# Kernel optimization log

Measured on AMD Instinct MI355X. Metric: run time of the kernel, lower is better.

The kernel has to match this reference:

```python
import jax, jax.numpy as jnp
import numpy as np

B = 16384
NUM_INPUTS = 256
ACTION_DIM = 16
H0 = 1024
H1 = 1024
K = 128  # num_support
MIN_BIN_WIDTH = 0.001
MIN_BIN_HEIGHT = 0.001
MIN_DERIVATIVE = 0.001
EDGE_CONST = float(np.log(np.exp(1.0 - 0.001) - 1.0))  # log(exp(0.999)-1)
LN_EPS = 1e-5


def setup_inputs() -> dict:
    key = jax.random.key(0)
    ks = jax.random.split(key, 16)
    def lin(kw, kb, fan_out, fan_in):
        w = 1.0 / np.sqrt(fan_in)
        W = jax.random.uniform(kw, (fan_out, fan_in), jnp.float32, -w, w)
        b = jax.random.uniform(kb, (fan_out,), jnp.float32, -w, w)
        return W, b
    w1, b1 = lin(ks[0], ks[1], H0, NUM_INPUTS)
    w2, b2 = lin(ks[2], ks[3], H1, H0 + ACTION_DIM)
    wv, bv = lin(ks[4], ks[5], 3 * K - 1, H1)
    wa = jax.random.uniform(ks[6], (1, H1), jnp.float32, -0.003, 0.003)
    ba = jax.random.uniform(ks[7], (1,), jnp.float32, -0.0003, 0.0003)
    wb = jax.random.uniform(ks[8], (1, H1), jnp.float32, -0.003, 0.003)
    bb = jax.random.uniform(ks[9], (1,), jnp.float32, -0.0003, 0.0003)
    return {
        "inputs": jax.random.normal(ks[10], (B, NUM_INPUTS), jnp.float32),
        "actions": jax.random.normal(ks[11], (B, ACTION_DIM), jnp.float32),
        "w1": w1, "b1": b1,
        "ln1_g": jnp.ones((H0,), jnp.float32), "ln1_b": jnp.zeros((H0,), jnp.float32),
        "w2": w2, "b2": b2,
        "ln2_g": jnp.ones((H1,), jnp.float32), "ln2_b": jnp.zeros((H1,), jnp.float32),
        "wv": wv, "bv": bv,
        "wa": wa, "ba": ba,
        "wb": wb, "bb": bb,
    }


def _layernorm(x, g, b):
    mu = jnp.mean(x, axis=-1, keepdims=True)
    var = jnp.mean((x - mu) ** 2, axis=-1, keepdims=True)
    return (x - mu) / jnp.sqrt(var + LN_EPS) * g + b


def reference(inputs, actions, w1, b1, ln1_g, ln1_b, w2, b2, ln2_g, ln2_b,
              wv, bv, wa, ba, wb, bb):
    # trunk MLP
    x = jax.nn.relu(_layernorm(inputs @ w1.T + b1, ln1_g, ln1_b))
    x = jnp.concatenate([x, actions], axis=1)
    x = jax.nn.relu(_layernorm(x @ w2.T + b2, ln2_g, ln2_b))

    spline_param = x @ wv.T + bv            # [B, 3K-1]
    scale_a = jnp.exp(x @ wa.T + ba)        # [B, 1]
    scale_b = x @ wb.T + bb                 # [B, 1]

    W = spline_param[:, :K]
    H = spline_param[:, K:2 * K]
    Draw = spline_param[:, 2 * K:]          # [B, K-1]

    W = MIN_BIN_WIDTH + (1 - MIN_BIN_WIDTH * K) * jax.nn.softmax(W, axis=1)
    H = MIN_BIN_HEIGHT + (1 - MIN_BIN_HEIGHT * K) * jax.nn.softmax(H, axis=1)
    Dmid = MIN_DERIVATIVE + jax.nn.softplus(Draw)
    edge = jnp.full((W.shape[0], 1), EDGE_CONST, W.dtype)
    D = jnp.concatenate([edge, Dmid, edge], axis=-1)  # [B, K+1]

    zeros = jnp.zeros((W.shape[0], 1), W.dtype)
    cumwidths = jnp.concatenate([zeros, jnp.cumsum(W, axis=-1)], axis=-1)
    cumwidths = cumwidths.at[..., -1].set(1.0)        # [B, K+1]
    widths = cumwidths[..., 1:] - cumwidths[..., :-1]

    cumheights = jnp.concatenate([zeros, jnp.cumsum(H, axis=-1)], axis=-1)
    cumheights = scale_a * cumheights + scale_b       # [B, K+1]
    heights = cumheights[..., 1:] - cumheights[..., :-1]

    tau = (jnp.arange(K, dtype=W.dtype) + 0.5) / K    # [K]

    # brute-force searchsorted: sum(tau >= cumwidths) - 1
    bin_idx = jnp.sum(tau[None, :, None] >= cumwidths[:, None, :], axis=-1) - 1  # [B,K]

    gather = lambda t: jnp.take_along_axis(t, bin_idx, axis=-1)
    input_cumwidths = gather(cumwidths)
    input_bin_widths = gather(widths)
    input_cumheights = gather(cumheights)
    input_heights = gather(heights)
    delta = heights / widths
    input_delta = gather(delta)
    input_derivatives = gather(D)
    input_derivatives_plus_one = gather(D[..., 1:])

    theta = (tau[None, :] - input_cumwidths) / input_bin_widths
    theta_one_minus = theta * (1 - theta)
    numerator = input_heights * (input_delta * theta ** 2 + input_derivatives * theta_one_minus)
    denominator = input_delta + (input_derivatives + input_derivatives_plus_one - 2 * input_delta) * theta_one_minus
    return input_cumheights + numerator / denominator  # [B, K]
```

## Files before the change

### kernel.cpp

```cpp
#include <hip/hip_runtime.h>
#include <hip/hip_bf16.h>
#include <math.h>

#define BROWS      16384
#define LN_EPS_F   1e-5f
#define MINW       0.001f
#define MINH       0.001f
#define MIND       0.001f
#define EDGE_CONST_F 0.5397423505783211f

typedef __bf16 bf16x8 __attribute__((ext_vector_type(8)));
typedef float  f32x4  __attribute__((ext_vector_type(4)));

__device__ __forceinline__ ushort f2bf(float x) {
    union { float f; unsigned u; } v; v.f = x;
    unsigned u = v.u;
    u += 0x7fffu + ((u >> 16) & 1u);
    return (ushort)(u >> 16);
}
__device__ __forceinline__ float bf2f(ushort h) {
    union { unsigned u; float f; } v; v.u = ((unsigned)h) << 16;
    return v.f;
}

__global__ __launch_bounds__(256, 2)
void gemm_bf16x3(const ushort* __restrict__ Ah, const ushort* __restrict__ Al,
                 const ushort* __restrict__ Bh, const ushort* __restrict__ Bl,
                 const float* __restrict__ bias,
                 float* __restrict__ C, int ldc, int Nstore, int Kpad)
{
    __shared__ ushort lds[32768];
    const int tid  = threadIdx.x;
    const int wid  = tid >> 6;
    const int lane = tid & 63;
    const int bm0  = blockIdx.x * 128;
    const int bn0  = blockIdx.y * 128;
    const int wm   = wid >> 1;
    const int wn   = wid & 1;
    const int l15  = lane & 15;
    const int kg   = lane >> 4;

    const ushort* gsrc[8];
    {
        const ushort* pb[4] = {Ah, Al, Bh, Bl};
        #pragma unroll
        for (int i = 0; i < 8; ++i) {
            const int F     = i * 4096 + tid * 16;
            const int pl    = F >> 13;
            const int chunk = (F & 8191) >> 4;
            const int kgrp  = chunk >> 7;
            const int row   = chunk & 127;
            const int r0    = (pl < 2) ? bm0 : bn0;
            gsrc[i] = pb[pl] + (size_t)(r0 + row) * Kpad + kgrp * 8;
        }
    }
    #define STAGE(bufbase, kelem)                                              \
        _Pragma("unroll")                                                      \
        for (int i = 0; i < 8; ++i) {                                          \
            __builtin_amdgcn_global_load_lds(                                  \
                (const __attribute__((address_space(1))) void*)(gsrc[i] + (kelem)), \
                (__attribute__((address_space(3))) void*)(&lds[(bufbase) + i * 2048 + wid * 512]), \
                16, 0, 0);                                                     \
        }

    f32x4 acc[4][4];
    #pragma unroll
    for (int m = 0; m < 4; ++m)
        #pragma unroll
        for (int n = 0; n < 4; ++n)
            acc[m][n] = (f32x4){0.f, 0.f, 0.f, 0.f};

    const int aoff = kg * 1024 + (wm * 64 + l15) * 8;
    const int boff = 8192 + kg * 1024 + (wn * 64 + l15) * 8;
    const int nt = Kpad >> 5;

    STAGE(0, 0);
    __syncthreads();
    int cur = 0;

    for (int t = 0; t < nt; ++t) {
        const int nxt = cur ^ 1;
        if (t + 1 < nt) STAGE(nxt * 16384, (t + 1) * 32);

        const int cb = cur * 16384;
        bf16x8 aH[4], aL[4], bH[4], bL[4];
        #pragma unroll
        for (int m = 0; m < 4; ++m) {
            aH[m] = *(const bf16x8*)&lds[cb + aoff + m * 128];
            aL[m] = *(const bf16x8*)&lds[cb + 4096 + aoff + m * 128];
        }
        #pragma unroll
        for (int n = 0; n < 4; ++n) {
            bH[n] = *(const bf16x8*)&lds[cb + boff + n * 128];
            bL[n] = *(const bf16x8*)&lds[cb + 4096 + boff + n * 128];
        }

        __builtin_amdgcn_s_setprio(1);
        #pragma unroll
        for (int m = 0; m < 4; ++m)
            #pragma unroll
            for (int n = 0; n < 4; ++n)
                acc[m][n] = __builtin_amdgcn_mfma_f32_16x16x32_bf16(aH[m], bH[n], acc[m][n], 0, 0, 0);
        #pragma unroll
        for (int m = 0; m < 4; ++m)
            #pragma unroll
            for (int n = 0; n < 4; ++n)
                acc[m][n] = __builtin_amdgcn_mfma_f32_16x16x32_bf16(aH[m], bL[n], acc[m][n], 0, 0, 0);
        #pragma unroll
        for (int m = 0; m < 4; ++m)
            #pragma unroll
            for (int n = 0; n < 4; ++n)
                acc[m][n] = __builtin_amdgcn_mfma_f32_16x16x32_bf16(aL[m], bH[n], acc[m][n], 0, 0, 0);
        __builtin_amdgcn_s_setprio(0);

        __syncthreads();
        cur = nxt;
    }
    #undef STAGE

    #pragma unroll
    for (int n = 0; n < 4; ++n) {
        const int col = bn0 + wn * 64 + n * 16 + l15;
        if (col < Nstore) {
            const float bs = bias[col];
            #pragma unroll
            for (int m = 0; m < 4; ++m) {
                const int row = bm0 + wm * 64 + m * 16 + kg * 4;
                #pragma unroll
                for (int r = 0; r < 4; ++r)
                    C[(size_t)(row + r) * ldc + col] = acc[m][n][r] + bs;
            }
        }
    }
}

__global__ __launch_bounds__(256)
void ln_relu_split(const float* __restrict__ Y,
                   const float* __restrict__ g, const float* __restrict__ b,
                   ushort* __restrict__ Xh, ushort* __restrict__ Xl, int xstride,
                   const float* __restrict__ actions, int dopad)
{
    __shared__ float red[4];
    const int row = blockIdx.x;
    const int tid = threadIdx.x;
    const float* y = Y + (size_t)row * 1024;

    const float4 v = *(const float4*)(y + tid * 4);
    float s = v.x + v.y + v.z + v.w;
    #pragma unroll
    for (int off = 32; off > 0; off >>= 1) s += __shfl_down(s, off, 64);
    if ((tid & 63) == 0) red[tid >> 6] = s;
    __syncthreads();
    const float mu = (red[0] + red[1] + red[2] + red[3]) * (1.f / 1024.f);
    __syncthreads();
    const float d0 = v.x - mu, d1 = v.y - mu, d2 = v.z - mu, d3 = v.w - mu;
    float s2 = d0 * d0 + d1 * d1 + d2 * d2 + d3 * d3;
    #pragma unroll
    for (int off = 32; off > 0; off >>= 1) s2 += __shfl_down(s2, off, 64);
    if ((tid & 63) == 0) red[tid >> 6] = s2;
    __syncthreads();
    const float var = (red[0] + red[1] + red[2] + red[3]) * (1.f / 1024.f);
    const float inv = 1.0f / sqrtf(var + LN_EPS_F);

    float o0 = fmaxf(0.f, d0 * inv * g[tid * 4 + 0] + b[tid * 4 + 0]);
    float o1 = fmaxf(0.f, d1 * inv * g[tid * 4 + 1] + b[tid * 4 + 1]);
    float o2 = fmaxf(0.f, d2 * inv * g[tid * 4 + 2] + b[tid * 4 + 2]);
    float o3 = fmaxf(0.f, d3 * inv * g[tid * 4 + 3] + b[tid * 4 + 3]);

    ushort4 oh, ol;
    oh.x = f2bf(o0); ol.x = f2bf(o0 - bf2f(oh.x));
    oh.y = f2bf(o1); ol.y = f2bf(o1 - bf2f(oh.y));
    oh.z = f2bf(o2); ol.z = f2bf(o2 - bf2f(oh.z));
    oh.w = f2bf(o3); ol.w = f2bf(o3 - bf2f(oh.w));
    *(ushort4*)(Xh + (size_t)row * xstride + tid * 4) = oh;
    *(ushort4*)(Xl + (size_t)row * xstride + tid * 4) = ol;

    if (actions != nullptr && tid < 16) {
        const float a = actions[(size_t)row * 16 + tid];
        const ushort h = f2bf(a);
        Xh[(size_t)row * xstride + 1024 + tid] = h;
        Xl[(size_t)row * xstride + 1024 + tid] = f2bf(a - bf2f(h));
    }
    if (dopad && tid >= 16 && tid < 64) {
        Xh[(size_t)row * xstride + 1024 + tid] = 0;
        Xl[(size_t)row * xstride + 1024 + tid] = 0;
    }
}

__global__ __launch_bounds__(256)
void split_mat(const float* __restrict__ src, int scols,
               ushort* __restrict__ Dh, ushort* __restrict__ Dl,
               int dcols, int total)
{
    const int idx = blockIdx.x * 256 + threadIdx.x;
    if (idx >= total) return;
    const int r = idx / dcols, c = idx % dcols;
    const float v = (c < scols) ? src[(size_t)r * scols + c] : 0.f;
    const ushort h = f2bf(v);
    Dh[idx] = h;
    Dl[idx] = f2bf(v - bf2f(h));
}

__global__ __launch_bounds__(256)
void build_wcat_split(const float* __restrict__ wv, const float* __restrict__ wa,
                      const float* __restrict__ wb, const float* __restrict__ bv,
                      const float* __restrict__ ba, const float* __restrict__ bb,
                      ushort* __restrict__ Wh, ushort* __restrict__ Wl,
                      float* __restrict__ bcat)
{
    const int idx = blockIdx.x * 256 + threadIdx.x;
    if (idx < 512 * 1024) {
        const int n = idx >> 10, k = idx & 1023;
        const float v = (n < 383) ? wv[n * 1024 + k]
                       : (n == 383) ? wa[k]
                       : (n == 384) ? wb[k] : 0.f;
        const ushort h = f2bf(v);
        Wh[idx] = h;
        Wl[idx] = f2bf(v - bf2f(h));
    }
    if (idx < 512) {
        bcat[idx] = (idx < 383) ? bv[idx] : (idx == 383) ? ba[0]
                   : (idx == 384) ? bb[0] : 0.f;
    }
}

__device__ __forceinline__ float softplus_f(float x) {
    return (x > 20.f) ? x : log1pf(expf(x));
}

__global__ __launch_bounds__(256)
void spline_rq(const float* __restrict__ P, float* __restrict__ Out)
{
    __shared__ float cw[4][132];
    __shared__ float ch[4][132];
    __shared__ float Dv[4][132];
    const int wid  = threadIdx.x >> 6;
    const int lane = threadIdx.x & 63;
    const int r    = blockIdx.x * 4 + wid;
    const float* p = P + (size_t)r * 385;
    const int e0 = 2 * lane, e1 = 2 * lane + 1;

    const float sa = expf(p[383]);
    const float sb = p[384];

    const float w0 = p[e0], w1 = p[e1];
    float mx = fmaxf(w0, w1);
    #pragma unroll
    for (int off = 1; off < 64; off <<= 1) mx = fmaxf(mx, __shfl_xor(mx, off, 64));
    const float xw0 = expf(w0 - mx), xw1 = expf(w1 - mx);
    float sw = xw0 + xw1;
    #pragma unroll
    for (int off = 1; off < 64; off <<= 1) sw += __shfl_xor(sw, off, 64);
    const float cwn = (1.f - MINW * 128.f) / sw;
    const float Wv0 = MINW + cwn * xw0;
    const float Wv1 = MINW + cwn * xw1;
    float s = Wv0 + Wv1;
    #pragma unroll
    for (int off = 1; off < 64; off <<= 1) {
        const float t = __shfl_up(s, off, 64);
        if (lane >= off) s += t;
    }
    if (lane == 0) cw[wid][0] = 0.f;
    cw[wid][e1]     = s - Wv1;
    cw[wid][e1 + 1] = (lane == 63) ? 1.0f : s;

    const float h0 = p[128 + e0], h1 = p[128 + e1];
    float mh = fmaxf(h0, h1);
    #pragma unroll
    for (int off = 1; off < 64; off <<= 1) mh = fmaxf(mh, __shfl_xor(mh, off, 64));
    const float xh0 = expf(h0 - mh), xh1 = expf(h1 - mh);
    float sh = xh0 + xh1;
    #pragma unroll
    for (int off = 1; off < 64; off <<= 1) sh += __shfl_xor(sh, off, 64);
    const float chn = (1.f - MINH * 128.f) / sh;
    const float Hv0 = MINH + chn * xh0;
    const float Hv1 = MINH + chn * xh1;
    float t2 = Hv0 + Hv1;
    #pragma unroll
    for (int off = 1; off < 64; off <<= 1) {
        const float t = __shfl_up(t2, off, 64);
        if (lane >= off) t2 += t;
    }
    if (lane == 0) ch[wid][0] = sb;
    ch[wid][e1]     = sa * (t2 - Hv1) + sb;
    ch[wid][e1 + 1] = sa * t2 + sb;

    if (lane == 0) { Dv[wid][0] = EDGE_CONST_F; Dv[wid][128] = EDGE_CONST_F; }
    Dv[wid][e0 + 1] = MIND + softplus_f(p[256 + e0]);
    if (lane < 63) Dv[wid][e1 + 1] = MIND + softplus_f(p[256 + e1]);

    __syncthreads();

    #pragma unroll
    for (int t = 0; t < 2; ++t) {
        const int e = 2 * lane + t;
        const float tau = ((float)e + 0.5f) * (1.f / 128.f);
        int lo = 0, hi = 128;
        #pragma unroll
        for (int it = 0; it < 7; ++it) {
            const int mid = (lo + hi) >> 1;
            if (cw[wid][mid] <= tau) lo = mid; else hi = mid;
        }
        const int bin = lo;
        const float icw = cw[wid][bin];
        const float ibw = cw[wid][bin + 1] - icw;
        const float ich = ch[wid][bin];
        const float ih  = ch[wid][bin + 1] - ich;
        const float idelta = ih / ibw;
        const float dd0 = Dv[wid][bin];
        const float dd1 = Dv[wid][bin + 1];
        const float theta = (tau - icw) / ibw;
        const float tom = theta * (1.f - theta);
        const float num = ih * (idelta * theta * theta + dd0 * tom);
        const float den = idelta + (dd0 + dd1 - 2.f * idelta) * tom;
        Out[(size_t)r * 128 + e] = ich + num / den;
    }
}

extern "C" void kernel_launch(void* const* d_in, const int* in_sizes, int n_in,
                              void* d_out, int out_size, void* d_ws, size_t ws_size,
                              hipStream_t stream) {
    const float* inputs  = (const float*)d_in[0];
    const float* actions = (const float*)d_in[1];
    const float* w1      = (const float*)d_in[2];
    const float* b1      = (const float*)d_in[3];
    const float* ln1_g   = (const float*)d_in[4];
    const float* ln1_b   = (const float*)d_in[5];
    const float* w2      = (const float*)d_in[6];
    const float* b2      = (const float*)d_in[7];
    const float* ln2_g   = (const float*)d_in[8];
    const float* ln2_b   = (const float*)d_in[9];
    const float* wv      = (const float*)d_in[10];
    const float* bv      = (const float*)d_in[11];
    const float* wa      = (const float*)d_in[12];
    const float* ba      = (const float*)d_in[13];
    const float* wb      = (const float*)d_in[14];
    const float* bb      = (const float*)d_in[15];

    float*  ws_y  = (float*)d_ws;
    ushort* ws_Xh = (ushort*)(ws_y + (size_t)16384 * 1024);
    ushort* ws_Xl = ws_Xh + (size_t)16384 * 1088;
    ushort* w1h   = ws_Xl + (size_t)16384 * 1088;
    ushort* w1l   = w1h + 1024 * 256;
    ushort* w2h   = w1l + 1024 * 256;
    ushort* w2l   = w2h + 1024 * 1088;
    ushort* wch   = w2l + 1024 * 1088;
    ushort* wcl   = wch + 512 * 1024;
    float*  bcat  = (float*)(wcl + 512 * 1024);

    split_mat<<<(16384 * 256 + 255) / 256, 256, 0, stream>>>(inputs, 256, ws_Xh, ws_Xl, 256, 16384 * 256);
    split_mat<<<(1024 * 256 + 255) / 256, 256, 0, stream>>>(w1, 256, w1h, w1l, 256, 1024 * 256);
    split_mat<<<(1024 * 1088 + 255) / 256, 256, 0, stream>>>(w2, 1040, w2h, w2l, 1088, 1024 * 1088);
    build_wcat_split<<<(512 * 1024 + 255) / 256, 256, 0, stream>>>(wv, wa, wb, bv, ba, bb, wch, wcl, bcat);

    gemm_bf16x3<<<dim3(128, 8), 256, 0, stream>>>(ws_Xh, ws_Xl, w1h, w1l, b1, ws_y, 1024, 1024, 256);
    ln_relu_split<<<16384, 256, 0, stream>>>(ws_y, ln1_g, ln1_b, ws_Xh, ws_Xl, 1088, actions, 1);

    gemm_bf16x3<<<dim3(128, 8), 256, 0, stream>>>(ws_Xh, ws_Xl, w2h, w2l, b2, ws_y, 1024, 1024, 1088);
    ln_relu_split<<<16384, 256, 0, stream>>>(ws_y, ln2_g, ln2_b, ws_Xh, ws_Xl, 1024, nullptr, 0);

    gemm_bf16x3<<<dim3(128, 4), 256, 0, stream>>>(ws_Xh, ws_Xl, wch, wcl, bcat, ws_y, 385, 385, 1024);

    spline_rq<<<4096, 256, 0, stream>>>(ws_y, (float*)d_out);
}
```

Measured before the change: 451.6 us.

## Use partial vmcnt waits for double-buffered GEMM and vectorize split_mat

The GEMM main loop replaces __syncthreads with explicit s_waitcnt vmcnt(8) plus s_barrier. Only the previous stage's global-to-LDS loads must land before compute, so the prefetch of the next tile stays in flight during the MFMAs. The split_mat kernel is also vectorized to process 4 elements per thread with float4 loads and ushort4 stores, cutting its thread count and memory transactions. The hand-written waitcnt depends on the exact count of outstanding loads issued by STAGE, and an undercount would read LDS data before it arrives.

```diff
diff --git a/kernel.cpp b/kernel.cpp
--- a/kernel.cpp
+++ b/kernel.cpp
@@ -75,12 +75,19 @@
     const int nt = Kpad >> 5;
 
     STAGE(0, 0);
-    __syncthreads();
     int cur = 0;
 
     for (int t = 0; t < nt; ++t) {
         const int nxt = cur ^ 1;
-        if (t + 1 < nt) STAGE(nxt * 16384, (t + 1) * 32);
+        if (t + 1 < nt) {
+            STAGE(nxt * 16384, (t + 1) * 32);
+            asm volatile("s_waitcnt vmcnt(8)" ::: "memory");
+        } else {
+            asm volatile("s_waitcnt vmcnt(0)" ::: "memory");
+        }
+        __builtin_amdgcn_sched_barrier(0);
+        __builtin_amdgcn_s_barrier();
+        asm volatile("" ::: "memory");
 
         const int cb = cur * 16384;
         bf16x8 aH[4], aL[4], bH[4], bL[4];
@@ -113,7 +120,10 @@
                 acc[m][n] = __builtin_amdgcn_mfma_f32_16x16x32_bf16(aL[m], bH[n], acc[m][n], 0, 0, 0);
         __builtin_amdgcn_s_setprio(0);
 
-        __syncthreads();
+        asm volatile("s_waitcnt lgkmcnt(0)" ::: "memory");
+        __builtin_amdgcn_sched_barrier(0);
+        __builtin_amdgcn_s_barrier();
+        asm volatile("" ::: "memory");
         cur = nxt;
     }
     #undef STAGE
@@ -192,13 +202,25 @@
                ushort* __restrict__ Dh, ushort* __restrict__ Dl,
                int dcols, int total)
 {
-    const int idx = blockIdx.x * 256 + threadIdx.x;
+    const int idx = (blockIdx.x * 256 + threadIdx.x) * 4;
     if (idx >= total) return;
     const int r = idx / dcols, c = idx % dcols;
-    const float v = (c < scols) ? src[(size_t)r * scols + c] : 0.f;
-    const ushort h = f2bf(v);
-    Dh[idx] = h;
-    Dl[idx] = f2bf(v - bf2f(h));
+    float e[4];
+    if (c + 3 < scols) {
+        const float4 v = *(const float4*)(src + (size_t)r * scols + c);
+        e[0] = v.x; e[1] = v.y; e[2] = v.z; e[3] = v.w;
+    } else {
+        #pragma unroll
+        for (int j = 0; j < 4; ++j)
+            e[j] = (c + j < scols) ? src[(size_t)r * scols + c + j] : 0.f;
+    }
+    ushort4 h, l;
+    h.x = f2bf(e[0]); l.x = f2bf(e[0] - bf2f(h.x));
+    h.y = f2bf(e[1]); l.y = f2bf(e[1] - bf2f(h.y));
+    h.z = f2bf(e[2]); l.z = f2bf(e[2] - bf2f(h.z));
+    h.w = f2bf(e[3]); l.w = f2bf(e[3] - bf2f(h.w));
+    *(ushort4*)(Dh + idx) = h;
+    *(ushort4*)(Dl + idx) = l;
 }
 
 __global__ __launch_bounds__(256)
@@ -348,9 +370,9 @@
     ushort* wcl   = wch + 512 * 1024;
     float*  bcat  = (float*)(wcl + 512 * 1024);
 
-    split_mat<<<(16384 * 256 + 255) / 256, 256, 0, stream>>>(inputs, 256, ws_Xh, ws_Xl, 256, 16384 * 256);
-    split_mat<<<(1024 * 256 + 255) / 256, 256, 0, stream>>>(w1, 256, w1h, w1l, 256, 1024 * 256);
-    split_mat<<<(1024 * 1088 + 255) / 256, 256, 0, stream>>>(w2, 1040, w2h, w2l, 1088, 1024 * 1088);
+    split_mat<<<(16384 * 256 / 4 + 255) / 256, 256, 0, stream>>>(inputs, 256, ws_Xh, ws_Xl, 256, 16384 * 256);
+    split_mat<<<(1024 * 256 / 4 + 255) / 256, 256, 0, stream>>>(w1, 256, w1h, w1l, 256, 1024 * 256);
+    split_mat<<<(1024 * 1088 / 4 + 255) / 256, 256, 0, stream>>>(w2, 1040, w2h, w2l, 1088, 1024 * 1088);
     build_wcat_split<<<(512 * 1024 + 255) / 256, 256, 0, stream>>>(wv, wa, wb, bv, ba, bb, wch, wcl, bcat);
 
     gemm_bf16x3<<<dim3(128, 8), 256, 0, stream>>>(ws_Xh, ws_Xl, w1h, w1l, b1, ws_y, 1024, 1024, 256);
```

Result: faster. 432.6 us (-4.2%).
